# Kernel optimization log

Measured on AMD Instinct MI355X. Metric: run time of the kernel, lower is better.

## Reference

```python
import jax, jax.numpy as jnp
import numpy as np

K = 16        # max_points
S = 3         # num_scales
D_MODEL = 256
KDIM = 16
TAU = 1e-4
B_BATCH = 512


def _boundaries(k):
    edges = [(i, j) for i in range(k) for j in range(i + 1, k)]
    tris = [(i, j, kk) for i in range(k) for j in range(i + 1, k) for kk in range(j + 1, k)]
    E, T = len(edges), len(tris)
    B1 = np.zeros((k, E), np.float32)
    for e, (i, j) in enumerate(edges):
        B1[i, e] = -1.0
        B1[j, e] = 1.0
    e2i = {e: idx for idx, e in enumerate(edges)}
    B2 = np.zeros((E, T), np.float32)
    for t, (i, j, kk) in enumerate(tris):
        B2[e2i[(j, kk)], t] = 1.0
        B2[e2i[(i, kk)], t] = -1.0
        B2[e2i[(i, j)], t] = 1.0
    e_i = np.array([e[0] for e in edges], np.int32)
    e_j = np.array([e[1] for e in edges], np.int32)
    t_ij = np.array([e2i[(a, b)] for (a, b, c) in tris], np.int32)
    t_jk = np.array([e2i[(b, c)] for (a, b, c) in tris], np.int32)
    t_ik = np.array([e2i[(a, c)] for (a, b, c) in tris], np.int32)
    return B1, B2, e_i, e_j, t_ij, t_jk, t_ik


def setup_inputs() -> dict:
    key = jax.random.key(0)
    ks = jax.random.split(key, 8)
    d = D_MODEL
    B1, B2, e_i, e_j, t_ij, t_jk, t_ik = _boundaries(K)

    def lin(kk, fin, fout):
        return jax.random.normal(kk, (fin, fout), jnp.float32) / np.sqrt(fin).astype(np.float32)

    return dict(
        x=jax.random.normal(ks[0], (B_BATCH, K, d), jnp.float32),
        mask=jnp.ones((B_BATCH, K), jnp.float32),
        B1=jnp.asarray(B1), B2=jnp.asarray(B2), abs_B1=jnp.asarray(np.abs(B1)),
        e_i=jnp.asarray(e_i), e_j=jnp.asarray(e_j),
        t_ij=jnp.asarray(t_ij), t_jk=jnp.asarray(t_jk), t_ik=jnp.asarray(t_ik),
        log_scales=jnp.linspace(-1.5, 1.5, S).astype(jnp.float32),
        Wg=lin(ks[1], d, KDIM), bg=jnp.zeros((KDIM,), jnp.float32),
        Wv0=lin(ks[2], d, d * S), bv0=jnp.zeros((d * S,), jnp.float32),
        We=lin(ks[3], d, d * S), be=jnp.zeros((d * S,), jnp.float32),
        Wout=lin(ks[4], 2 * S * d, d), bout=jnp.zeros((d,), jnp.float32),
        g1=jnp.ones((d,), jnp.float32), b1=jnp.zeros((d,), jnp.float32),
        g2=jnp.ones((d,), jnp.float32), b2=jnp.zeros((d,), jnp.float32),
        Wf1=lin(ks[5], d, 4 * d), bf1=jnp.zeros((4 * d,), jnp.float32),
        Wf2=lin(ks[6], 4 * d, d), bf2=jnp.zeros((d,), jnp.float32),
    )


def _layernorm(x, g, b):
    mu = jnp.mean(x, -1, keepdims=True)
    var = jnp.mean(jnp.square(x - mu), -1, keepdims=True)
    return (x - mu) * jax.lax.rsqrt(var + 1e-5) * g + b


def _forward(x, mask, B1, B2, abs_B1, e_i, e_j, t_ij, t_jk, t_ik,
             log_scales, Wg, bg, Wv0, bv0, We, be, Wout, bout,
             g1, b1, g2, b2, Wf1, bf1, Wf2, bf2):
    B, Kp, d = x.shape
    E = B1.shape[1]
    residual = x
    x_norm = _layernorm(x, g1, b1)
    P = x_norm @ Wg + bg                                   # (B,K,k_dim)
    mask2 = mask[:, :, None] * mask[:, None, :]            # (B,K,K)
    # cdist (safe sqrt: zero diag, no NaN grads)
    pn = jnp.sum(P * P, -1)
    d2 = jnp.maximum(pn[:, :, None] + pn[:, None, :] - 2.0 * jnp.einsum('bik,bjk->bij', P, P), 0.0)
    Dm = jnp.where(d2 > 0, jnp.sqrt(jnp.where(d2 > 0, d2, 1.0)), 0.0) * mask2
    sigma_sq = jnp.square(jnp.exp(log_scales))             # (S,)
    A = jnp.exp(-(Dm * Dm)[:, None] / (2.0 * sigma_sq[None, :, None, None] + 1e-8)) * mask2[:, None]  # (B,S,K,K)
    W1 = A[:, :, e_i, e_j]                                 # (B,S,E) edge gather
    W2 = W1[:, :, t_ij] * W1[:, :, t_jk] * W1[:, :, t_ik]  # (B,S,T) triangle weights
    V0 = (x_norm @ Wv0 + bv0).reshape(B, Kp, S, d).transpose(0, 2, 1, 3)         # (B,S,K,d)
    E_raw = jnp.einsum('ke,bkd->bed', abs_B1, x_norm)                            # (B,E,d)
    E_in = (E_raw @ We + be).reshape(B, E, S, d).transpose(0, 2, 1, 3)           # (B,S,E,d)
    # L0 = B1 diag(W1) B1^T + tau I
    L0 = jnp.einsum('ke,bse,me->bskm', B1, W1, B1) + TAU * jnp.eye(Kp, dtype=x.dtype)
    M0 = jnp.einsum('bskm,bsmd->bskd', L0, V0)
    # L1 = B1^T diag(mask) B1 + B2 diag(W2) B2^T + tau I
    term_down = jnp.einsum('ke,bk,kf->bef', B1, mask, B1)                        # (B,E,E)
    term_up = jnp.einsum('et,bst,ft->bsef', B2, W2, B2)                          # (B,S,E,E)
    L1 = term_down[:, None] + term_up + TAU * jnp.eye(E, dtype=x.dtype)
    M1 = jnp.einsum('bsef,bsfd->bsed', L1, E_in)
    M1n = jnp.einsum('ke,bsed->bskd', abs_B1, M1)                                # edges -> nodes
    node_cat = M0.transpose(0, 2, 1, 3).reshape(B, Kp, S * d)
    edge_cat = M1n.transpose(0, 2, 1, 3).reshape(B, Kp, S * d)
    attn = jnp.concatenate([node_cat, edge_cat], -1) @ Wout + bout
    x2 = residual + attn                                   # dropout is identity in eval
    h = jax.nn.gelu(_layernorm(x2, g2, b2) @ Wf1 + bf1, approximate=False) @ Wf2 + bf2
    return x2 + h


def reference(x, mask, B1, B2, abs_B1, e_i, e_j, t_ij, t_jk, t_ik,
              log_scales, Wg, bg, Wv0, bv0, We, be, Wout, bout,
              g1, b1, g2, b2, Wf1, bf1, Wf2, bf2):
    return _forward(x, mask, B1, B2, abs_B1, e_i, e_j, t_ij, t_jk, t_ik,
                    log_scales, Wg, bg, Wv0, bv0, We, be, Wout, bout,
                    g1, b1, g2, b2, Wf1, bf1, Wf2, bf2)
```

## Files before the change

### kernel.cpp

```cpp
#include <hip/hip_runtime.h>
#include <math.h>

#define KN 16
#define DM 256
#define NS 3
#define NE 120
#define NT_TRI 560
#define NBATCH 512
#define TAUF 1e-4f
#define KAUG 1600

typedef unsigned short ushort_t;
typedef __attribute__((ext_vector_type(8))) short short8v;
typedef __attribute__((ext_vector_type(4))) short short4v;
typedef __attribute__((ext_vector_type(4))) float f32x4;

#define OFF_WSTACK 0u
#define OFF_WF1T   819200u
#define OFF_WF2T   1343488u
#define OFF_Z      1867776u
#define OFF_H      1867776u
#define OFF_LN2    28082176u

__device__ __forceinline__ ushort_t f2bf(float f) {
    union { float f; unsigned int u; } v; v.f = f;
    unsigned int r = v.u + 0x7FFFu + ((v.u >> 16) & 1u);
    return (ushort_t)(r >> 16);
}
__device__ __forceinline__ void gload_lds16(const void* g, void* l) {
    auto gp = (const __attribute__((address_space(1))) unsigned int*)(unsigned long long)(g);
    auto lp = (__attribute__((address_space(3))) unsigned int*)(unsigned long long)(l);
    __builtin_amdgcn_global_load_lds(gp, lp, 16, 0, 0);
}

__global__ __launch_bounds__(256) void prep_kernel(
    const float* __restrict__ Wv0, const float* __restrict__ bv0,
    const float* __restrict__ We,  const float* __restrict__ be,
    const float* __restrict__ Wout,
    const float* __restrict__ Wf1, const float* __restrict__ Wf2,
    ushort_t* __restrict__ wstack, ushort_t* __restrict__ wf1t,
    ushort_t* __restrict__ wf2t)
{
    __shared__ float lhs[16][DM];
    __shared__ float tile[64][65];
    const int bid = blockIdx.x;
    const int j = threadIdx.x;

    if (bid < 102) {
        const int m = bid / 17, by = bid % 17;
        const int path = m / 3, s = m % 3;
        const float* __restrict__ Wo = Wout + (size_t)m*DM*DM;
        if (by == 16) {
            const float* bv = (path == 0) ? bv0 : be;
            const float f = (path == 0) ? 1.0f : 0.5f;
            float acc = 0.f;
            for (int k = 0; k < DM; ++k)
                acc += bv[s*DM + k] * f * Wo[k*DM + j];
            wstack[(size_t)j*KAUG + 1536 + m] = f2bf(acc);
            if (m == 0)
                for (int c = 1542; c < KAUG; ++c)
                    wstack[(size_t)j*KAUG + c] = 0;
            return;
        }
        const float* src = (path == 0) ? Wv0 : We;
        const int i0 = by * 16;
        for (int r = 0; r < 16; ++r)
            lhs[r][j] = src[(size_t)(i0 + r)*(NS*DM) + s*DM + j];
        __syncthreads();
        float acc[16];
#pragma unroll
        for (int r = 0; r < 16; ++r) acc[r] = 0.f;
        for (int k = 0; k < DM; ++k) {
            const float w = Wo[k*DM + j];
#pragma unroll
            for (int r = 0; r < 16; ++r) acc[r] += lhs[r][k] * w;
        }
#pragma unroll
        for (int r = 0; r < 16; ++r)
            wstack[(size_t)j*KAUG + m*DM + i0 + r] = f2bf(acc[r]);
        return;
    }

    const float* in; ushort_t* outp; int R, C, rt, ct;
    if (bid < 166) {
        const int q = bid - 102;
        in = Wf1; outp = wf1t; R = 256; C = 1024;
        rt = (q >> 4) * 64; ct = (q & 15) * 64;
    } else {
        const int q = bid - 166;
        in = Wf2; outp = wf2t; R = 1024; C = 256;
        rt = (q >> 2) * 64; ct = (q & 3) * 64;
    }
#pragma unroll
    for (int q2 = 0; q2 < 16; ++q2) {
        const int idx = q2*256 + j;
        const int r = idx >> 6, c = idx & 63;
        tile[r][c] = in[(size_t)(rt + r)*C + ct + c];
    }
    __syncthreads();
#pragma unroll
    for (int q2 = 0; q2 < 16; ++q2) {
        const int idx = q2*256 + j;
        const int cc = idx >> 6, rr = idx & 63;
        outp[(size_t)(ct + cc)*R + rt + rr] = f2bf(tile[rr][cc]);
    }
}

__global__ __launch_bounds__(256) void attn_topo_kernel(
    const float* __restrict__ x, const float* __restrict__ mask,
    const int* __restrict__ e_i, const int* __restrict__ e_j,
    const int* __restrict__ t_ij, const int* __restrict__ t_jk, const int* __restrict__ t_ik,
    const float* __restrict__ log_scales,
    const float* __restrict__ Wg, const float* __restrict__ bg,
    const float* __restrict__ g1, const float* __restrict__ b1,
    ushort_t* __restrict__ Z)
{
    const int b = blockIdx.x;
    const int t = threadIdx.x;

    __shared__ ushort_t xnb[KN][DM];
    __shared__ float Plds[KN][KN];
    __shared__ float pn[KN];
    __shared__ float msk[KN];
    __shared__ float sA[NS][KN][KN];
    __shared__ int   eidx[KN][KN];
    __shared__ float Qm[KN][KN];
    __shared__ float P2m[KN][KN];
    __shared__ float HQ[KN][KN];
    __shared__ float Hup[NS][KN][KN];
    __shared__ float Tm[2*NS][KN][20];

    const int r  = t >> 4;
    const int cg = (t & 15) * 16;

    float xv[16];
    {
        const float* xr = x + (size_t)(b*KN + r)*DM + cg;
        float ssum = 0.f;
#pragma unroll
        for (int q = 0; q < 16; ++q) { xv[q] = xr[q]; ssum += xv[q]; }
#pragma unroll
        for (int o = 1; o < 16; o <<= 1) ssum += __shfl_xor(ssum, o);
        const float mu = ssum * (1.f/DM);
        float vsum = 0.f;
#pragma unroll
        for (int q = 0; q < 16; ++q) { float d = xv[q]-mu; vsum += d*d; }
#pragma unroll
        for (int o = 1; o < 16; o <<= 1) vsum += __shfl_xor(vsum, o);
        const float rstd = rsqrtf(vsum*(1.f/DM) + 1e-5f);
        short8v o0, o1;
#pragma unroll
        for (int q = 0; q < 16; ++q) {
            const int c = cg + q;
            xv[q] = (xv[q]-mu)*rstd*g1[c] + b1[c];
            if (q < 8) o0[q] = (short)f2bf(xv[q]); else o1[q-8] = (short)f2bf(xv[q]);
        }
        *(short8v*)&xnb[r][cg]     = o0;
        *(short8v*)&xnb[r][cg+8]   = o1;
        if (t < KN) msk[t] = mask[b*KN + t];
    }

    {
        float part[16];
#pragma unroll
        for (int c = 0; c < 16; ++c) part[c] = 0.f;
#pragma unroll
        for (int q = 0; q < 16; ++q) {
            const float xq = xv[q];
            const float* wr = Wg + (size_t)(cg + q)*KN;
            const f32x4 w0 = *(const f32x4*)(wr);
            const f32x4 w1 = *(const f32x4*)(wr + 4);
            const f32x4 w2 = *(const f32x4*)(wr + 8);
            const f32x4 w3 = *(const f32x4*)(wr + 12);
            part[0]  += xq*w0[0]; part[1]  += xq*w0[1]; part[2]  += xq*w0[2]; part[3]  += xq*w0[3];
            part[4]  += xq*w1[0]; part[5]  += xq*w1[1]; part[6]  += xq*w1[2]; part[7]  += xq*w1[3];
            part[8]  += xq*w2[0]; part[9]  += xq*w2[1]; part[10] += xq*w2[2]; part[11] += xq*w2[3];
            part[12] += xq*w3[0]; part[13] += xq*w3[1]; part[14] += xq*w3[2]; part[15] += xq*w3[3];
        }
        const int b0 = t & 1, b1b = (t>>1)&1, b2 = (t>>2)&1, b3 = (t>>3)&1;
        float p8[8];
#pragma unroll
        for (int c2 = 0; c2 < 8; ++c2) {
            const float keep = b0 ? part[2*c2+1] : part[2*c2];
            const float send = b0 ? part[2*c2]   : part[2*c2+1];
            p8[c2] = keep + __shfl_xor(send, 1);
        }
        float p4[4];
#pragma unroll
        for (int c2 = 0; c2 < 4; ++c2) {
            const float keep = b1b ? p8[2*c2+1] : p8[2*c2];
            const float send = b1b ? p8[2*c2]   : p8[2*c2+1];
            p4[c2] = keep + __shfl_xor(send, 2);
        }
        float p2v[2];
#pragma unroll
        for (int c2 = 0; c2 < 2; ++c2) {
            const float keep = b2 ? p4[2*c2+1] : p4[2*c2];
            const float send = b2 ? p4[2*c2]   : p4[2*c2+1];
            p2v[c2] = keep + __shfl_xor(send, 4);
        }
        {
            const float keep = b3 ? p2v[1] : p2v[0];
            const float send = b3 ? p2v[0] : p2v[1];
            Plds[r][t & 15] = keep + __shfl_xor(send, 8) + bg[t & 15];
        }
    }
    __syncthreads();
    if (t < KN) {
        float s = 0.f;
#pragma unroll
        for (int k = 0; k < KN; ++k) { const float p = Plds[t][k]; s += p*p; }
        pn[t] = s;
    }
    __syncthreads();

    {
        const int rr = t & 15, c = t >> 4;
        float dot = 0.f;
#pragma unroll
        for (int k = 0; k < KN; ++k) dot += Plds[rr][k]*Plds[c][k];
        float d2 = pn[rr] + pn[c] - 2.f*dot;
        const float m2 = msk[rr]*msk[c];
        const float dm = (d2 > 0.f) ? sqrtf(d2)*m2 : 0.f;
        const float dmsq = dm*dm;
#pragma unroll
        for (int s = 0; s < NS; ++s) {
            const float sig2 = expf(2.f*log_scales[s]);
            sA[s][rr][c] = expf(-dmsq/(2.f*sig2 + 1e-8f)) * m2;
        }
        eidx[rr][c] = -1;
    }
    __syncthreads();
    if (t < NE) {
        const int i = e_i[t], jn = e_j[t];
        eidx[i][jn] = t; eidx[jn][i] = t;
    }
    __syncthreads();

    {
        const int n = t & 15, mcol = t >> 4;
        float q, p2;
        if (n != mcol) {
            const int e = eidx[n][mcol];
            if (e >= 0) { q = (mcol == e_j[e]) ? 1.f : -1.f; p2 = 1.f; }
            else        { q = 0.f; p2 = 0.f; }
        } else {
            q = 0.f; p2 = 0.f;
            for (int kk = 0; kk < KN; ++kk) {
                if (kk == n) continue;
                const int e = eidx[n][kk];
                if (e >= 0) { q += (n == e_j[e]) ? 1.f : -1.f; p2 += 1.f; }
            }
        }
        Qm[n][mcol] = q; P2m[n][mcol] = p2;
#pragma unroll
        for (int s = 0; s < NS; ++s) {
            float v;
            if (n != mcol) v = (eidx[n][mcol] >= 0) ? -sA[s][n][mcol] : 0.f;
            else {
                v = TAUF;
                for (int kk = 0; kk < KN; ++kk)
                    if (kk != n && eidx[n][kk] >= 0) v += sA[s][n][kk];
            }
            Tm[s][n][mcol] = v;
            Hup[s][n][mcol] = 0.f;
        }
    }
    __syncthreads();
    {
        const int n = t & 15, mcol = t >> 4;
        float acc = 0.f;
#pragma unroll
        for (int kk = 0; kk < KN; ++kk) acc += msk[kk]*Qm[n][kk]*Qm[mcol][kk];
        HQ[n][mcol] = acc;
    }
    for (int tt = t; tt < NT_TRI; tt += 256) {
        const int eij = t_ij[tt], ejk = t_jk[tt], eik = t_ik[tt];
        const int a0 = e_i[eij], a1 = e_j[eij];
        const int b0 = e_i[ejk], b1_ = e_j[ejk];
        const int c0 = e_i[eik], c1 = e_j[eik];
        float wprod[NS];
#pragma unroll
        for (int s = 0; s < NS; ++s)
            wprod[s] = sA[s][a0][a1] * sA[s][b0][b1_] * sA[s][c0][c1];
        int un[6]; int nu = 0;
        const int nodes[6] = {a0,a1,b0,b1_,c0,c1};
        for (int ii = 0; ii < 6; ++ii) {
            const int nd = nodes[ii]; bool seen = false;
            for (int jj = 0; jj < nu; ++jj) if (un[jj] == nd) seen = true;
            if (!seen) un[nu++] = nd;
        }
        float cf[6];
        for (int ii = 0; ii < nu; ++ii) {
            const int nd = un[ii];
            float c = 0.f;
            if (nd==b0 || nd==b1_) c += 1.f;
            if (nd==c0 || nd==c1 ) c -= 1.f;
            if (nd==a0 || nd==a1 ) c += 1.f;
            cf[ii] = c;
        }
        for (int ii = 0; ii < nu; ++ii) {
            if (cf[ii] == 0.f) continue;
            for (int jj = 0; jj < nu; ++jj) {
                if (cf[jj] == 0.f) continue;
                const float cc = cf[ii]*cf[jj];
#pragma unroll
                for (int s = 0; s < NS; ++s)
                    atomicAdd(&Hup[s][un[ii]][un[jj]], cc*wprod[s]);
            }
        }
    }
    __syncthreads();
    {
        const int n = t & 15, mcol = t >> 4;
#pragma unroll
        for (int s = 0; s < NS; ++s)
            Tm[NS+s][n][mcol] = HQ[n][mcol] + Hup[s][n][mcol] + TAUF*P2m[n][mcol];
    }
    __syncthreads();

    {
        ushort_t* Zb = Z + (size_t)b*KN*KAUG;
        const int w = t >> 6, l = t & 63;
        const int lr = l & 15, lk = l >> 4;

        if (t < 96) {
            const int m6 = t >> 4, n = t & 15;
            float s = 0.f;
#pragma unroll
            for (int mm = 0; mm < KN; ++mm) s += Tm[m6][n][mm];
            Zb[(size_t)n*KAUG + 1536 + m6] = f2bf(s);
        }
        for (int idx = t; idx < 16*58; idx += 256) {
            const int n = idx / 58, c = 1542 + idx % 58;
            Zb[(size_t)n*KAUG + c] = 0;
        }

        short8v bfr[4];
#pragma unroll
        for (int q4 = 0; q4 < 4; ++q4) {
            const int jc = w*64 + q4*16 + lr;
#pragma unroll
            for (int i = 0; i < 8; ++i)
                bfr[q4][i] = (lk < 2) ? (short)xnb[lk*8 + i][jc] : (short)0;
        }
#pragma unroll
        for (int m6 = 0; m6 < 6; ++m6) {
            short8v af = {0,0,0,0,0,0,0,0};
            if (lk < 2) {
                const f32x4 t0 = *(const f32x4*)&Tm[m6][lr][lk*8];
                const f32x4 t1 = *(const f32x4*)&Tm[m6][lr][lk*8 + 4];
                af[0] = (short)f2bf(t0[0]); af[1] = (short)f2bf(t0[1]);
                af[2] = (short)f2bf(t0[2]); af[3] = (short)f2bf(t0[3]);
                af[4] = (short)f2bf(t1[0]); af[5] = (short)f2bf(t1[1]);
                af[6] = (short)f2bf(t1[2]); af[7] = (short)f2bf(t1[3]);
            }
#pragma unroll
            for (int q4 = 0; q4 < 4; ++q4) {
                f32x4 acc = {0.f,0.f,0.f,0.f};
                acc = __builtin_amdgcn_mfma_f32_16x16x32_bf16(af, bfr[q4], acc, 0, 0, 0);
                const int jc = w*64 + q4*16 + lr;
#pragma unroll
                for (int rg = 0; rg < 4; ++rg) {
                    const int n = lk*4 + rg;
                    Zb[(size_t)n*KAUG + m6*256 + jc] = f2bf(acc[rg]);
                }
            }
        }
    }
}

template<int BM, int BN, int KD, int EPI>
__global__ __launch_bounds__(256) void gemm_lds(
    const ushort_t* __restrict__ A, const ushort_t* __restrict__ Bt,
    const float* __restrict__ bias, const float* __restrict__ resid,
    float* __restrict__ outF, ushort_t* __restrict__ outH, int ldo)
{
    constexpr int BK = 64;
    constexpr int MF = BM / 32, NF = BN / 32;
    __shared__ ushort_t lA[BM*BK];
    __shared__ ushort_t lB[BN*BK];
    const int t = threadIdx.x;
    const int w = t >> 6, l = t & 63;
    const int wm = w & 1, wn = w >> 1;
    const int lr = l & 15, lk = l >> 4;
    const int brow = blockIdx.x * BM;
    const int bcol = blockIdx.y * BN;

    f32x4 acc[MF][NF];
#pragma unroll
    for (int mf = 0; mf < MF; ++mf)
#pragma unroll
        for (int nt = 0; nt < NF; ++nt)
            acc[mf][nt] = (f32x4){0.f,0.f,0.f,0.f};

    const int byteoff = t * 16;

    for (int kc = 0; kc < KD/BK; ++kc) {
        if (kc) __syncthreads();
#pragma unroll
        for (int c = 0; c < BM/32; ++c) {
            const int bo = c*4096 + byteoff;
            const int row = bo >> 7, kb = bo & 127;
            gload_lds16(A + (size_t)(brow + row)*KD + kc*BK + (kb >> 1), lA + (bo >> 1));
        }
#pragma unroll
        for (int c = 0; c < BN/32; ++c) {
            const int bo = c*4096 + byteoff;
            const int row = bo >> 7, kb = bo & 127;
            gload_lds16(Bt + (size_t)(bcol + row)*KD + kc*BK + (kb >> 1), lB + (bo >> 1));
        }
        __syncthreads();
#pragma unroll
        for (int ks = 0; ks < 2; ++ks) {
            short8v af[MF], bfr[NF];
#pragma unroll
            for (int mf = 0; mf < MF; ++mf)
                af[mf] = *(const short8v*)(lA + (wm*(BM/2) + mf*16 + lr)*BK + ks*32 + lk*8);
#pragma unroll
            for (int nt = 0; nt < NF; ++nt)
                bfr[nt] = *(const short8v*)(lB + (wn*(BN/2) + nt*16 + lr)*BK + ks*32 + lk*8);
#pragma unroll
            for (int mf = 0; mf < MF; ++mf)
#pragma unroll
                for (int nt = 0; nt < NF; ++nt)
                    acc[mf][nt] = __builtin_amdgcn_mfma_f32_16x16x32_bf16(
                        af[mf], bfr[nt], acc[mf][nt], 0, 0, 0);
        }
    }

#pragma unroll
    for (int mf = 0; mf < MF; ++mf) {
#pragma unroll
        for (int nt = 0; nt < NF; ++nt) {
            const int col = bcol + wn*(BN/2) + nt*16 + lr;
#pragma unroll
            for (int rg = 0; rg < 4; ++rg) {
                const int row = brow + wm*(BM/2) + mf*16 + lk*4 + rg;
                const size_t o = (size_t)row * ldo + col;
                const float v = acc[mf][nt][rg];
                if (EPI == 1) {
                    const float u = v + bias[col];
                    const float a = 0.79788456080286536f*(u + 0.044715f*u*u*u);
                    outH[o] = f2bf(u / (1.f + __expf(-2.f*a)));
                } else if (EPI == 2) {
                    outF[o] = outF[o] + v + bias[col];
                } else {
                    outF[o] = resid[o] + v + bias[col];
                }
            }
        }
    }
}

__global__ __launch_bounds__(256) void ln_rows_kernel(
    const float* __restrict__ in, const float* __restrict__ g,
    const float* __restrict__ bvec, ushort_t* __restrict__ outv)
{
    const int row = blockIdx.x*4 + (threadIdx.x >> 6);
    const int l = threadIdx.x & 63;
    const float4 v = *(const float4*)(in + (size_t)row*DM + l*4);
    float s = v.x + v.y + v.z + v.w;
#pragma unroll
    for (int o = 1; o < 64; o <<= 1) s += __shfl_xor(s, o);
    const float mu = s * (1.f/DM);
    float d0 = v.x-mu, d1 = v.y-mu, d2 = v.z-mu, d3 = v.w-mu;
    float vs = d0*d0 + d1*d1 + d2*d2 + d3*d3;
#pragma unroll
    for (int o = 1; o < 64; o <<= 1) vs += __shfl_xor(vs, o);
    const float rstd = rsqrtf(vs*(1.f/DM) + 1e-5f);
    short4v o4;
    o4[0] = (short)f2bf(d0*rstd*g[l*4+0] + bvec[l*4+0]);
    o4[1] = (short)f2bf(d1*rstd*g[l*4+1] + bvec[l*4+1]);
    o4[2] = (short)f2bf(d2*rstd*g[l*4+2] + bvec[l*4+2]);
    o4[3] = (short)f2bf(d3*rstd*g[l*4+3] + bvec[l*4+3]);
    *(short4v*)(outv + (size_t)row*DM + l*4) = o4;
}

extern "C" void kernel_launch(void* const* d_in, const int* in_sizes, int n_in,
                              void* d_out, int out_size, void* d_ws, size_t ws_size,
                              hipStream_t stream) {
    const float* x          = (const float*)d_in[0];
    const float* mask       = (const float*)d_in[1];
    const int*   e_i        = (const int*)  d_in[5];
    const int*   e_j        = (const int*)  d_in[6];
    const int*   t_ij       = (const int*)  d_in[7];
    const int*   t_jk       = (const int*)  d_in[8];
    const int*   t_ik       = (const int*)  d_in[9];
    const float* log_scales = (const float*)d_in[10];
    const float* Wg         = (const float*)d_in[11];
    const float* bg         = (const float*)d_in[12];
    const float* Wv0        = (const float*)d_in[13];
    const float* bv0        = (const float*)d_in[14];
    const float* We         = (const float*)d_in[15];
    const float* be         = (const float*)d_in[16];
    const float* Wout       = (const float*)d_in[17];
    const float* bout       = (const float*)d_in[18];
    const float* g1         = (const float*)d_in[19];
    const float* b1         = (const float*)d_in[20];
    const float* g2         = (const float*)d_in[21];
    const float* b2         = (const float*)d_in[22];
    const float* Wf1        = (const float*)d_in[23];
    const float* bf1        = (const float*)d_in[24];
    const float* Wf2        = (const float*)d_in[25];
    const float* bf2        = (const float*)d_in[26];

    char* wsb = (char*)d_ws;
    ushort_t* wstack = (ushort_t*)(wsb + OFF_WSTACK);
    ushort_t* wf1t   = (ushort_t*)(wsb + OFF_WF1T);
    ushort_t* wf2t   = (ushort_t*)(wsb + OFF_WF2T);
    ushort_t* Z      = (ushort_t*)(wsb + OFF_Z);
    ushort_t* H      = (ushort_t*)(wsb + OFF_H);
    ushort_t* ln2    = (ushort_t*)(wsb + OFF_LN2);
    float*    out    = (float*)d_out;

    hipLaunchKernelGGL(prep_kernel, dim3(230), dim3(256), 0, stream,
                       Wv0, bv0, We, be, Wout, Wf1, Wf2, wstack, wf1t, wf2t);
    hipLaunchKernelGGL(attn_topo_kernel, dim3(NBATCH), dim3(256), 0, stream,
                       x, mask, e_i, e_j, t_ij, t_jk, t_ik, log_scales,
                       Wg, bg, g1, b1, Z);
    hipLaunchKernelGGL((gemm_lds<64,64,KAUG,3>), dim3(128,4), dim3(256), 0, stream,
                       Z, wstack, bout, x, out, (ushort_t*)nullptr, 256);
    hipLaunchKernelGGL(ln_rows_kernel, dim3(2048), dim3(256), 0, stream,
                       out, g2, b2, ln2);
    hipLaunchKernelGGL((gemm_lds<128,128,256,1>), dim3(64,8), dim3(256), 0, stream,
                       ln2, wf1t, bf1, (const float*)nullptr,
                       (float*)nullptr, H, 1024);
    hipLaunchKernelGGL((gemm_lds<64,64,1024,2>), dim3(128,4), dim3(256), 0, stream,
                       H, wf2t, bf2, (const float*)nullptr,
                       out, (ushort_t*)nullptr, 256);
}
```

Measured before the change: 131.4 us.

## Precompute topology tables once and simplify per-batch Hodge assembly in attn kernel

Moves construction of the edge-index, incidence-derived Q/P2/adjacency matrices and packed triangle vertex lists into an extra prep block, so they are built once rather than in each of the 512 batch blocks. The triangle up-Laplacian contribution is reduced to a diagonal-only atomic update at each triangle's middle node, replacing the per-triangle node dedup and outer-product atomics. It also computes pairwise distances directly, builds the bf16 MFMA operands in LDS during assembly, transposes the LN output in LDS for vector B-fragment loads, and uses vector loads for x, g1 and b1. It depends on the algebraic claim that only the middle-node diagonal survives, and it adds an extra prep block plus a dependency on workspace tables.

```diff
diff --git a/kernel.cpp b/kernel.cpp
--- a/kernel.cpp
+++ b/kernel.cpp
@@ -18,9 +18,10 @@
 #define OFF_WSTACK 0u
 #define OFF_WF1T   819200u
 #define OFF_WF2T   1343488u
-#define OFF_Z      1867776u
-#define OFF_H      1867776u
-#define OFF_LN2    28082176u
+#define OFF_TOPO   1867776u
+#define OFF_Z      1875968u
+#define OFF_H      1875968u
+#define OFF_LN2    28090368u
 
 __device__ __forceinline__ ushort_t f2bf(float f) {
     union { float f; unsigned int u; } v; v.f = f;
@@ -38,13 +39,52 @@
     const float* __restrict__ We,  const float* __restrict__ be,
     const float* __restrict__ Wout,
     const float* __restrict__ Wf1, const float* __restrict__ Wf2,
+    const int* __restrict__ e_i, const int* __restrict__ e_j,
+    const int* __restrict__ t_ij, const int* __restrict__ t_jk, const int* __restrict__ t_ik,
     ushort_t* __restrict__ wstack, ushort_t* __restrict__ wf1t,
-    ushort_t* __restrict__ wf2t)
+    ushort_t* __restrict__ wf2t,
+    float* __restrict__ topoF, int* __restrict__ triPk)
 {
     __shared__ float lhs[16][DM];
     __shared__ float tile[64][65];
+    __shared__ int   eidxL[256];
     const int bid = blockIdx.x;
     const int j = threadIdx.x;
+
+    if (bid == 230) {
+        eidxL[j] = -1;
+        __syncthreads();
+        if (j < NE) {
+            const int i = e_i[j], jn = e_j[j];
+            eidxL[i*16 + jn] = j; eidxL[jn*16 + i] = j;
+        }
+        __syncthreads();
+        const int n = j >> 4, m = j & 15;
+        float q, p2, adj;
+        if (n != m) {
+            const int e = eidxL[j];
+            if (e >= 0) { q = (m == e_j[e]) ? 1.f : -1.f; p2 = 1.f; adj = 1.f; }
+            else        { q = 0.f; p2 = 0.f; adj = 0.f; }
+        } else {
+            q = 0.f; p2 = 0.f; adj = 0.f;
+            for (int kk = 0; kk < KN; ++kk) {
+                if (kk == n) continue;
+                const int e = eidxL[n*16 + kk];
+                if (e >= 0) { q += (n == e_j[e]) ? 1.f : -1.f; p2 += 1.f; }
+            }
+        }
+        topoF[j] = q; topoF[256 + j] = p2; topoF[512 + j] = adj;
+        for (int tt = j; tt < NT_TRI; tt += 256) {
+            const int eij = t_ij[tt], ejk = t_jk[tt], eik = t_ik[tt];
+            const int a0 = e_i[eij], a1 = e_j[eij];
+            const int b0 = e_i[ejk], b1v = e_j[ejk];
+            const int c0 = e_i[eik], c1 = e_j[eik];
+            const int mid = (b0 == a0 || b0 == a1) ? b0 : b1v;
+            triPk[2*tt]   = a0 | (a1 << 8) | (b0 << 16) | (b1v << 24);
+            triPk[2*tt+1] = c0 | (c1 << 8) | (mid << 16);
+        }
+        return;
+    }
 
     if (bid < 102) {
         const int m = bid / 17, by = bid % 17;
@@ -108,62 +148,75 @@
 
 __global__ __launch_bounds__(256) void attn_topo_kernel(
     const float* __restrict__ x, const float* __restrict__ mask,
-    const int* __restrict__ e_i, const int* __restrict__ e_j,
-    const int* __restrict__ t_ij, const int* __restrict__ t_jk, const int* __restrict__ t_ik,
     const float* __restrict__ log_scales,
     const float* __restrict__ Wg, const float* __restrict__ bg,
     const float* __restrict__ g1, const float* __restrict__ b1,
+    const float* __restrict__ topoF, const int* __restrict__ triPk,
     ushort_t* __restrict__ Z)
 {
     const int b = blockIdx.x;
     const int t = threadIdx.x;
-
-    __shared__ ushort_t xnb[KN][DM];
+    const int n = t >> 4, m = t & 15;
+
+    __shared__ ushort_t xnbT[DM][16];
     __shared__ float Plds[KN][KN];
-    __shared__ float pn[KN];
-    __shared__ float msk[KN];
+    __shared__ float mskL[KN];
+    __shared__ float QL[256];
+    __shared__ float P2L[256];
+    __shared__ float adjL[256];
     __shared__ float sA[NS][KN][KN];
-    __shared__ int   eidx[KN][KN];
-    __shared__ float Qm[KN][KN];
-    __shared__ float P2m[KN][KN];
-    __shared__ float HQ[KN][KN];
-    __shared__ float Hup[NS][KN][KN];
-    __shared__ float Tm[2*NS][KN][20];
-
-    const int r  = t >> 4;
-    const int cg = (t & 15) * 16;
+    __shared__ float Hupd[NS*KN];
+    __shared__ ushort_t Tbf[6][KN][32];
+
+    QL[t]  = topoF[t];
+    P2L[t] = topoF[256 + t];
+    adjL[t] = topoF[512 + t];
+    if (t < KN) mskL[t] = mask[b*KN + t];
 
     float xv[16];
     {
-        const float* xr = x + (size_t)(b*KN + r)*DM + cg;
+        const int cg = m * 16;
+        const float* xr = x + (size_t)(b*KN + n)*DM + cg;
+        const f32x4 v0 = *(const f32x4*)(xr);
+        const f32x4 v1 = *(const f32x4*)(xr + 4);
+        const f32x4 v2 = *(const f32x4*)(xr + 8);
+        const f32x4 v3 = *(const f32x4*)(xr + 12);
+#pragma unroll
+        for (int q = 0; q < 4; ++q) { xv[q] = v0[q]; xv[4+q] = v1[q]; xv[8+q] = v2[q]; xv[12+q] = v3[q]; }
         float ssum = 0.f;
 #pragma unroll
-        for (int q = 0; q < 16; ++q) { xv[q] = xr[q]; ssum += xv[q]; }
+        for (int q = 0; q < 16; ++q) ssum += xv[q];
 #pragma unroll
         for (int o = 1; o < 16; o <<= 1) ssum += __shfl_xor(ssum, o);
         const float mu = ssum * (1.f/DM);
         float vsum = 0.f;
 #pragma unroll
-        for (int q = 0; q < 16; ++q) { float d = xv[q]-mu; vsum += d*d; }
+        for (int q = 0; q < 16; ++q) { const float d = xv[q]-mu; vsum += d*d; }
 #pragma unroll
         for (int o = 1; o < 16; o <<= 1) vsum += __shfl_xor(vsum, o);
         const float rstd = rsqrtf(vsum*(1.f/DM) + 1e-5f);
-        short8v o0, o1;
+        const f32x4 ga = *(const f32x4*)(g1 + cg),   gb = *(const f32x4*)(g1 + cg + 4);
+        const f32x4 gc = *(const f32x4*)(g1 + cg + 8), gd = *(const f32x4*)(g1 + cg + 12);
+        const f32x4 ba = *(const f32x4*)(b1 + cg),   bb = *(const f32x4*)(b1 + cg + 4);
+        const f32x4 bc = *(const f32x4*)(b1 + cg + 8), bd = *(const f32x4*)(b1 + cg + 12);
+        float gg[16], bbv[16];
+#pragma unroll
+        for (int q = 0; q < 4; ++q) {
+            gg[q] = ga[q]; gg[4+q] = gb[q]; gg[8+q] = gc[q]; gg[12+q] = gd[q];
+            bbv[q] = ba[q]; bbv[4+q] = bb[q]; bbv[8+q] = bc[q]; bbv[12+q] = bd[q];
+        }
 #pragma unroll
         for (int q = 0; q < 16; ++q) {
-            const int c = cg + q;
-            xv[q] = (xv[q]-mu)*rstd*g1[c] + b1[c];
-            if (q < 8) o0[q] = (short)f2bf(xv[q]); else o1[q-8] = (short)f2bf(xv[q]);
-        }
-        *(short8v*)&xnb[r][cg]     = o0;
-        *(short8v*)&xnb[r][cg+8]   = o1;
-        if (t < KN) msk[t] = mask[b*KN + t];
+            xv[q] = (xv[q]-mu)*rstd*gg[q] + bbv[q];
+            xnbT[cg + q][n] = f2bf(xv[q]);
+        }
     }
 
     {
         float part[16];
 #pragma unroll
         for (int c = 0; c < 16; ++c) part[c] = 0.f;
+        const int cg = m * 16;
 #pragma unroll
         for (int q = 0; q < 16; ++q) {
             const float xq = xv[q];
@@ -199,172 +252,109 @@
             const float send = b2 ? p4[2*c2]   : p4[2*c2+1];
             p2v[c2] = keep + __shfl_xor(send, 4);
         }
-        {
-            const float keep = b3 ? p2v[1] : p2v[0];
-            const float send = b3 ? p2v[0] : p2v[1];
-            Plds[r][t & 15] = keep + __shfl_xor(send, 8) + bg[t & 15];
-        }
+        const float keep = b3 ? p2v[1] : p2v[0];
+        const float send = b3 ? p2v[0] : p2v[1];
+        Plds[n][m] = keep + __shfl_xor(send, 8) + bg[m];
     }
     __syncthreads();
-    if (t < KN) {
-        float s = 0.f;
-#pragma unroll
-        for (int k = 0; k < KN; ++k) { const float p = Plds[t][k]; s += p*p; }
-        pn[t] = s;
-    }
-    __syncthreads();
-
+
+    float T0[NS], hq;
     {
-        const int rr = t & 15, c = t >> 4;
-        float dot = 0.f;
-#pragma unroll
-        for (int k = 0; k < KN; ++k) dot += Plds[rr][k]*Plds[c][k];
-        float d2 = pn[rr] + pn[c] - 2.f*dot;
-        const float m2 = msk[rr]*msk[c];
-        const float dm = (d2 > 0.f) ? sqrtf(d2)*m2 : 0.f;
+        float d2 = 0.f;
+#pragma unroll
+        for (int k = 0; k < KN; ++k) {
+            const float dd = Plds[n][k] - Plds[m][k];
+            d2 += dd*dd;
+        }
+        const float m2v = mskL[n]*mskL[m];
+        const float dm = (d2 > 0.f) ? sqrtf(d2)*m2v : 0.f;
         const float dmsq = dm*dm;
+        const float adjv = adjL[t];
 #pragma unroll
         for (int s = 0; s < NS; ++s) {
             const float sig2 = expf(2.f*log_scales[s]);
-            sA[s][rr][c] = expf(-dmsq/(2.f*sig2 + 1e-8f)) * m2;
-        }
-        eidx[rr][c] = -1;
+            const float a = expf(-dmsq/(2.f*sig2 + 1e-8f)) * m2v;
+            sA[s][n][m] = a;
+            const float am = a * adjv;
+            float rsum = am;
+#pragma unroll
+            for (int o = 1; o < 16; o <<= 1) rsum += __shfl_xor(rsum, o);
+            const float tv = (m == n) ? (TAUF + rsum) : (-am);
+            T0[s] = tv;
+            Tbf[s][n][m] = f2bf(tv);
+        }
+        hq = 0.f;
+#pragma unroll
+        for (int k = 0; k < KN; ++k)
+            hq += mskL[k]*QL[n*16 + k]*QL[m*16 + k];
+        if (t < NS*KN) Hupd[t] = 0.f;
+#pragma unroll
+        for (int idx = 0; idx < 6; ++idx) {
+            const int e2 = idx*256 + t;
+            Tbf[e2 >> 8][(e2 >> 4) & 15][16 + (e2 & 15)] = 0;
+        }
     }
     __syncthreads();
-    if (t < NE) {
-        const int i = e_i[t], jn = e_j[t];
-        eidx[i][jn] = t; eidx[jn][i] = t;
+
+    for (int tt = t; tt < NT_TRI; tt += 256) {
+        const int w0 = triPk[2*tt], w1 = triPk[2*tt+1];
+        const int a0 = w0 & 255, a1 = (w0 >> 8) & 255;
+        const int b0 = (w0 >> 16) & 255, b1v = (w0 >> 24) & 255;
+        const int c0 = w1 & 255, c1 = (w1 >> 8) & 255, mid = (w1 >> 16) & 255;
+#pragma unroll
+        for (int s = 0; s < NS; ++s)
+            atomicAdd(&Hupd[s*KN + mid],
+                      4.f * sA[s][a0][a1] * sA[s][b0][b1v] * sA[s][c0][c1]);
     }
     __syncthreads();
 
+    ushort_t* Zb = Z + (size_t)b*KN*KAUG;
     {
-        const int n = t & 15, mcol = t >> 4;
-        float q, p2;
-        if (n != mcol) {
-            const int e = eidx[n][mcol];
-            if (e >= 0) { q = (mcol == e_j[e]) ? 1.f : -1.f; p2 = 1.f; }
-            else        { q = 0.f; p2 = 0.f; }
-        } else {
-            q = 0.f; p2 = 0.f;
-            for (int kk = 0; kk < KN; ++kk) {
-                if (kk == n) continue;
-                const int e = eidx[n][kk];
-                if (e >= 0) { q += (n == e_j[e]) ? 1.f : -1.f; p2 += 1.f; }
-            }
-        }
-        Qm[n][mcol] = q; P2m[n][mcol] = p2;
+        float T1[NS];
+        const float p2v = P2L[t];
 #pragma unroll
         for (int s = 0; s < NS; ++s) {
-            float v;
-            if (n != mcol) v = (eidx[n][mcol] >= 0) ? -sA[s][n][mcol] : 0.f;
-            else {
-                v = TAUF;
-                for (int kk = 0; kk < KN; ++kk)
-                    if (kk != n && eidx[n][kk] >= 0) v += sA[s][n][kk];
-            }
-            Tm[s][n][mcol] = v;
-            Hup[s][n][mcol] = 0.f;
+            const float tv = hq + TAUF*p2v + ((m == n) ? Hupd[s*KN + n] : 0.f);
+            T1[s] = tv;
+            Tbf[NS + s][n][m] = f2bf(tv);
+        }
+        float sv[6] = {T0[0], T0[1], T0[2], T1[0], T1[1], T1[2]};
+#pragma unroll
+        for (int q = 0; q < 6; ++q) {
+            float v = sv[q];
+#pragma unroll
+            for (int o = 1; o < 16; o <<= 1) v += __shfl_xor(v, o);
+            sv[q] = v;
+        }
+        const float wv = (m==0)?sv[0]:(m==1)?sv[1]:(m==2)?sv[2]:(m==3)?sv[3]:(m==4)?sv[4]:sv[5];
+        if (m < 6) Zb[(size_t)n*KAUG + 1536 + m] = f2bf(wv);
+        for (int idx = t; idx < 58*KN; idx += 256) {
+            const int nn = idx / 58, c = 1542 + idx % 58;
+            Zb[(size_t)nn*KAUG + c] = 0;
         }
     }
     __syncthreads();
+
     {
-        const int n = t & 15, mcol = t >> 4;
-        float acc = 0.f;
-#pragma unroll
-        for (int kk = 0; kk < KN; ++kk) acc += msk[kk]*Qm[n][kk]*Qm[mcol][kk];
-        HQ[n][mcol] = acc;
-    }
-    for (int tt = t; tt < NT_TRI; tt += 256) {
-        const int eij = t_ij[tt], ejk = t_jk[tt], eik = t_ik[tt];
-        const int a0 = e_i[eij], a1 = e_j[eij];
-        const int b0 = e_i[ejk], b1_ = e_j[ejk];
-        const int c0 = e_i[eik], c1 = e_j[eik];
-        float wprod[NS];
-#pragma unroll
-        for (int s = 0; s < NS; ++s)
-            wprod[s] = sA[s][a0][a1] * sA[s][b0][b1_] * sA[s][c0][c1];
-        int un[6]; int nu = 0;
-        const int nodes[6] = {a0,a1,b0,b1_,c0,c1};
-        for (int ii = 0; ii < 6; ++ii) {
-            const int nd = nodes[ii]; bool seen = false;
-            for (int jj = 0; jj < nu; ++jj) if (un[jj] == nd) seen = true;
-            if (!seen) un[nu++] = nd;
-        }
-        float cf[6];
-        for (int ii = 0; ii < nu; ++ii) {
-            const int nd = un[ii];
-            float c = 0.f;
-            if (nd==b0 || nd==b1_) c += 1.f;
-            if (nd==c0 || nd==c1 ) c -= 1.f;
-            if (nd==a0 || nd==a1 ) c += 1.f;
-            cf[ii] = c;
-        }
-        for (int ii = 0; ii < nu; ++ii) {
-            if (cf[ii] == 0.f) continue;
-            for (int jj = 0; jj < nu; ++jj) {
-                if (cf[jj] == 0.f) continue;
-                const float cc = cf[ii]*cf[jj];
-#pragma unroll
-                for (int s = 0; s < NS; ++s)
-                    atomicAdd(&Hup[s][un[ii]][un[jj]], cc*wprod[s]);
-            }
-        }
-    }
-    __syncthreads();
-    {
-        const int n = t & 15, mcol = t >> 4;
-#pragma unroll
-        for (int s = 0; s < NS; ++s)
-            Tm[NS+s][n][mcol] = HQ[n][mcol] + Hup[s][n][mcol] + TAUF*P2m[n][mcol];
-    }
-    __syncthreads();
-
-    {
-        ushort_t* Zb = Z + (size_t)b*KN*KAUG;
         const int w = t >> 6, l = t & 63;
         const int lr = l & 15, lk = l >> 4;
-
-        if (t < 96) {
-            const int m6 = t >> 4, n = t & 15;
-            float s = 0.f;
-#pragma unroll
-            for (int mm = 0; mm < KN; ++mm) s += Tm[m6][n][mm];
-            Zb[(size_t)n*KAUG + 1536 + m6] = f2bf(s);
-        }
-        for (int idx = t; idx < 16*58; idx += 256) {
-            const int n = idx / 58, c = 1542 + idx % 58;
-            Zb[(size_t)n*KAUG + c] = 0;
-        }
-
         short8v bfr[4];
 #pragma unroll
         for (int q4 = 0; q4 < 4; ++q4) {
             const int jc = w*64 + q4*16 + lr;
-#pragma unroll
-            for (int i = 0; i < 8; ++i)
-                bfr[q4][i] = (lk < 2) ? (short)xnb[lk*8 + i][jc] : (short)0;
+            bfr[q4] = *(const short8v*)&xnbT[jc][(lk & 1)*8];
         }
 #pragma unroll
         for (int m6 = 0; m6 < 6; ++m6) {
-            short8v af = {0,0,0,0,0,0,0,0};
-            if (lk < 2) {
-                const f32x4 t0 = *(const f32x4*)&Tm[m6][lr][lk*8];
-                const f32x4 t1 = *(const f32x4*)&Tm[m6][lr][lk*8 + 4];
-                af[0] = (short)f2bf(t0[0]); af[1] = (short)f2bf(t0[1]);
-                af[2] = (short)f2bf(t0[2]); af[3] = (short)f2bf(t0[3]);
-                af[4] = (short)f2bf(t1[0]); af[5] = (short)f2bf(t1[1]);
-                af[6] = (short)f2bf(t1[2]); af[7] = (short)f2bf(t1[3]);
-            }
+            const short8v af = *(const short8v*)&Tbf[m6][lr][lk*8];
 #pragma unroll
             for (int q4 = 0; q4 < 4; ++q4) {
                 f32x4 acc = {0.f,0.f,0.f,0.f};
                 acc = __builtin_amdgcn_mfma_f32_16x16x32_bf16(af, bfr[q4], acc, 0, 0, 0);
                 const int jc = w*64 + q4*16 + lr;
 #pragma unroll
-                for (int rg = 0; rg < 4; ++rg) {
-                    const int n = lk*4 + rg;
-                    Zb[(size_t)n*KAUG + m6*256 + jc] = f2bf(acc[rg]);
-                }
+                for (int rg = 0; rg < 4; ++rg)
+                    Zb[(size_t)(lk*4 + rg)*KAUG + m6*256 + jc] = f2bf(acc[rg]);
             }
         }
     }
@@ -509,16 +499,19 @@
     ushort_t* wstack = (ushort_t*)(wsb + OFF_WSTACK);
     ushort_t* wf1t   = (ushort_t*)(wsb + OFF_WF1T);
     ushort_t* wf2t   = (ushort_t*)(wsb + OFF_WF2T);
+    float*    topoF  = (float*)   (wsb + OFF_TOPO);
+    int*      triPk  = (int*)     (wsb + OFF_TOPO + 3072);
     ushort_t* Z      = (ushort_t*)(wsb + OFF_Z);
     ushort_t* H      = (ushort_t*)(wsb + OFF_H);
     ushort_t* ln2    = (ushort_t*)(wsb + OFF_LN2);
     float*    out    = (float*)d_out;
 
-    hipLaunchKernelGGL(prep_kernel, dim3(230), dim3(256), 0, stream,
-                       Wv0, bv0, We, be, Wout, Wf1, Wf2, wstack, wf1t, wf2t);
+    hipLaunchKernelGGL(prep_kernel, dim3(231), dim3(256), 0, stream,
+                       Wv0, bv0, We, be, Wout, Wf1, Wf2,
+                       e_i, e_j, t_ij, t_jk, t_ik,
+                       wstack, wf1t, wf2t, topoF, triPk);
     hipLaunchKernelGGL(attn_topo_kernel, dim3(NBATCH), dim3(256), 0, stream,
-                       x, mask, e_i, e_j, t_ij, t_jk, t_ik, log_scales,
-                       Wg, bg, g1, b1, Z);
+                       x, mask, log_scales, Wg, bg, g1, b1, topoF, triPk, Z);
     hipLaunchKernelGGL((gemm_lds<64,64,KAUG,3>), dim3(128,4), dim3(256), 0, stream,
                        Z, wstack, bout, x, out, (ushort_t*)nullptr, 256);
     hipLaunchKernelGGL(ln_rows_kernel, dim3(2048), dim3(256), 0, stream,
```

After: 122.2 us. 1.08x faster.
